# Kernel optimization log

Measured on AMD Instinct MI355X. Metric: run time of the kernel, lower is better.

Reference implementation:

```python
import jax, jax.numpy as jnp
import numpy as np


def setup_inputs() -> dict:
    key = jax.random.key(0)
    kA, kJ, kB, kP, kM = jax.random.split(key, 5)
    b, h, s = 4, 16, 1024
    A = jax.random.normal(kA, (b, h, s, s), dtype=jnp.float32)
    J = jax.random.normal(kJ, (b, h, s, s), dtype=jnp.float32)
    B = jax.random.normal(kB, (b, h, s, s), dtype=jnp.float32)
    P = jax.random.normal(kP, (b, h, s, s), dtype=jnp.float32)
    mask = jax.random.normal(kM, (1, s, s), dtype=jnp.float32)
    return {"A": A, "J": J, "B": B, "P": P, "mask": mask}


def reference(A, J, B, P, mask):
    # qk = A @ J + B, scaled by sqrt(last dim)
    s = A.shape[-1]
    scale = 1.0 / jnp.sqrt(jnp.asarray(s, dtype=A.dtype))
    qk = (jnp.einsum('bhik,bhkj->bhij', A, J) + B) * scale
    # mask [1, S, S] broadcasts over batch and heads, as in the torch source
    qk = qk + mask
    attn = jax.nn.softmax(qk, axis=-1)
    return jnp.einsum('bhij,bhjk->bhik', attn, P)
```

## Files before the change

### kernel.cpp

```cpp
#include <hip/hip_runtime.h>
#include <hip/hip_bf16.h>
#include <cstdint>


typedef __bf16 bf16x8 __attribute__((ext_vector_type(8)));
typedef __bf16 bf16x4 __attribute__((ext_vector_type(4)));
typedef float f32x4 __attribute__((ext_vector_type(4)));

static constexpr int SS = 1024;
static constexpr int BH = 64;
static constexpr size_t SLICE = (size_t)SS * SS;

__device__ __forceinline__ void async16(void* lds, const void* g) {
    __builtin_amdgcn_global_load_lds(
        (__attribute__((address_space(1))) void*)(g),
        (__attribute__((address_space(3))) void*)(lds), 16, 0, 0);
}

__global__ __launch_bounds__(256) void cast_bf16(const float4* __restrict__ in,
                                                 bf16x4* __restrict__ out, int n4) {
    int i = blockIdx.x * 256 + threadIdx.x;
    if (i < n4) {
        float4 v = in[i];
        bf16x4 o = {(__bf16)v.x, (__bf16)v.y, (__bf16)v.z, (__bf16)v.w};
        out[i] = o;
    }
}

__global__ __launch_bounds__(256) void transpose_cast(const float* __restrict__ in,
                                                      __bf16* __restrict__ out) {
    __shared__ float tile[32][33];
    const int bh = blockIdx.z;
    const int r0 = blockIdx.y * 32, c0 = blockIdx.x * 32;
    const int t = threadIdx.x;
    const int tr = t >> 3, tc4 = (t & 7) * 4;
    const float4 v = *(const float4*)(in + (size_t)bh * SLICE + (size_t)(r0 + tr) * SS + c0 + tc4);
    tile[tr][tc4 + 0] = v.x;
    tile[tr][tc4 + 1] = v.y;
    tile[tr][tc4 + 2] = v.z;
    tile[tr][tc4 + 3] = v.w;
    __syncthreads();
    const int oc = t >> 3;
    const int orr = (t & 7) * 4;
    bf16x4 o = {(__bf16)tile[orr + 0][oc], (__bf16)tile[orr + 1][oc],
                (__bf16)tile[orr + 2][oc], (__bf16)tile[orr + 3][oc]};
    *(bf16x4*)(out + (size_t)bh * SLICE + (size_t)(c0 + oc) * SS + r0 + orr) = o;
}


__global__ __launch_bounds__(256) void gemm_scores(const __bf16* __restrict__ Ab,
                                                   const __bf16* __restrict__ Jt,
                                                   const float* __restrict__ Bm,
                                                   const float* __restrict__ mask,
                                                   float* __restrict__ scores) {
    __shared__ __align__(16) __bf16 As[128 * 32];
    __shared__ __align__(16) __bf16 Bs[128 * 32];
    const int tid = threadIdx.x, lane = tid & 63, w = tid >> 6;
    const int wm = w >> 1, wn = w & 1;
    const int l16 = lane & 15, l4 = lane >> 4;
    const int bh = blockIdx.z;
    const int i0 = blockIdx.y * 128, j0 = blockIdx.x * 128;
    const size_t bhoff = (size_t)bh * SLICE;

    const __bf16* Ag = Ab + bhoff + (size_t)(i0 + w * 32 + (lane >> 2)) * SS + (lane & 3) * 8;
    const __bf16* Bg = Jt + bhoff + (size_t)(j0 + w * 32 + (lane >> 2)) * SS + (lane & 3) * 8;
    char* lA0 = (char*)As + w * 2048 + lane * 16;
    char* lB0 = (char*)Bs + w * 2048 + lane * 16;
    const __bf16* ar = As + (wm * 64 + l16) * 32 + l4 * 8;
    const __bf16* br = Bs + (wn * 64 + l16) * 32 + l4 * 8;

    f32x4 acc[4][4] = {};
    for (int kt = 0; kt < SS / 32; ++kt) {
        async16(lA0, Ag); async16(lA0 + 1024, Ag + 16 * SS);
        async16(lB0, Bg); async16(lB0 + 1024, Bg + 16 * SS);
        Ag += 32; Bg += 32;
        __syncthreads();
        bf16x8 af[4], bfr[4];
#pragma unroll
        for (int mi = 0; mi < 4; ++mi) af[mi] = *(const bf16x8*)(ar + mi * 16 * 32);
#pragma unroll
        for (int ni = 0; ni < 4; ++ni) bfr[ni] = *(const bf16x8*)(br + ni * 16 * 32);
#pragma unroll
        for (int mi = 0; mi < 4; ++mi)
#pragma unroll
            for (int ni = 0; ni < 4; ++ni)
                acc[mi][ni] = __builtin_amdgcn_mfma_f32_16x16x32_bf16(af[mi], bfr[ni], acc[mi][ni], 0, 0, 0);
        __syncthreads();
    }
    const float sc = 0.03125f;
#pragma unroll
    for (int mi = 0; mi < 4; ++mi) {
#pragma unroll
        for (int r = 0; r < 4; ++r) {
            const int ig = i0 + wm * 64 + mi * 16 + l4 * 4 + r;
#pragma unroll
            for (int ni = 0; ni < 4; ++ni) {
                const int jg = j0 + wn * 64 + ni * 16 + l16;
                const size_t off = bhoff + (size_t)ig * SS + jg;
                scores[off] = (acc[mi][ni][r] + Bm[off]) * sc + mask[(size_t)ig * SS + jg];
            }
        }
    }
}

__global__ __launch_bounds__(256) void gemm_out(const __bf16* __restrict__ At,
                                                const __bf16* __restrict__ Pt,
                                                float* __restrict__ out) {
    __shared__ __align__(16) __bf16 As[128 * 32];
    __shared__ __align__(16) __bf16 Bs[128 * 32];
    const int tid = threadIdx.x, lane = tid & 63, w = tid >> 6;
    const int wm = w >> 1, wn = w & 1;
    const int l16 = lane & 15, l4 = lane >> 4;
    const int bh = blockIdx.z;
    const int i0 = blockIdx.y * 128, j0 = blockIdx.x * 128;
    const size_t bhoff = (size_t)bh * SLICE;

    const __bf16* Ag = At + bhoff + (size_t)(i0 + w * 32 + (lane >> 2)) * SS + (lane & 3) * 8;
    const __bf16* Bg = Pt + bhoff + (size_t)(j0 + w * 32 + (lane >> 2)) * SS + (lane & 3) * 8;
    char* lA0 = (char*)As + w * 2048 + lane * 16;
    char* lB0 = (char*)Bs + w * 2048 + lane * 16;
    const __bf16* ar = As + (wm * 64 + l16) * 32 + l4 * 8;
    const __bf16* br = Bs + (wn * 64 + l16) * 32 + l4 * 8;

    f32x4 acc[4][4] = {};
    for (int kt = 0; kt < SS / 32; ++kt) {
        async16(lA0, Ag); async16(lA0 + 1024, Ag + 16 * SS);
        async16(lB0, Bg); async16(lB0 + 1024, Bg + 16 * SS);
        Ag += 32; Bg += 32;
        __syncthreads();
        bf16x8 af[4], bfr[4];
#pragma unroll
        for (int mi = 0; mi < 4; ++mi) af[mi] = *(const bf16x8*)(ar + mi * 16 * 32);
#pragma unroll
        for (int ni = 0; ni < 4; ++ni) bfr[ni] = *(const bf16x8*)(br + ni * 16 * 32);
#pragma unroll
        for (int mi = 0; mi < 4; ++mi)
#pragma unroll
            for (int ni = 0; ni < 4; ++ni)
                acc[mi][ni] = __builtin_amdgcn_mfma_f32_16x16x32_bf16(af[mi], bfr[ni], acc[mi][ni], 0, 0, 0);
        __syncthreads();
    }
#pragma unroll
    for (int mi = 0; mi < 4; ++mi) {
#pragma unroll
        for (int r = 0; r < 4; ++r) {
            const int ig = i0 + wm * 64 + mi * 16 + l4 * 4 + r;
#pragma unroll
            for (int ni = 0; ni < 4; ++ni) {
                const int jg = j0 + wn * 64 + ni * 16 + l16;
                out[bhoff + (size_t)ig * SS + jg] = acc[mi][ni][r];
            }
        }
    }
}

__global__ __launch_bounds__(256) void softmax_rows(const float* __restrict__ scores,
                                                    __bf16* __restrict__ attn) {
    const size_t row = blockIdx.x;
    const int t = threadIdx.x;
    const int lane = t & 63, w = t >> 6;
    __shared__ float red[8];

    float4 v = *(const float4*)(scores + row * SS + t * 4);
    float m = fmaxf(fmaxf(v.x, v.y), fmaxf(v.z, v.w));
#pragma unroll
    for (int o = 32; o; o >>= 1) m = fmaxf(m, __shfl_down(m, o));
    if (lane == 0) red[w] = m;
    __syncthreads();
    const float bm = fmaxf(fmaxf(red[0], red[1]), fmaxf(red[2], red[3]));
    const float e0 = __expf(v.x - bm), e1 = __expf(v.y - bm);
    const float e2 = __expf(v.z - bm), e3 = __expf(v.w - bm);
    float s = e0 + e1 + e2 + e3;
#pragma unroll
    for (int o = 32; o; o >>= 1) s += __shfl_down(s, o);
    __syncthreads();
    if (lane == 0) red[4 + w] = s;
    __syncthreads();
    const float inv = 1.0f / (red[4] + red[5] + red[6] + red[7]);
    bf16x4 o = {(__bf16)(e0 * inv), (__bf16)(e1 * inv), (__bf16)(e2 * inv), (__bf16)(e3 * inv)};
    *(bf16x4*)(attn + row * SS + t * 4) = o;
}

extern "C" void kernel_launch(void* const* d_in, const int* in_sizes, int n_in,
                              void* d_out, int out_size, void* d_ws, size_t ws_size,
                              hipStream_t stream) {
    const float* A    = (const float*)d_in[0];
    const float* J    = (const float*)d_in[1];
    const float* Bm   = (const float*)d_in[2];
    const float* P    = (const float*)d_in[3];
    const float* mask = (const float*)d_in[4];
    float* out = (float*)d_out;

    char* ws = (char*)d_ws;
    const size_t MB128 = (size_t)128 * 1024 * 1024;
    __bf16* Ab   = (__bf16*)ws;
    __bf16* Jt   = (__bf16*)(ws + MB128);
    __bf16* Pt   = (__bf16*)(ws + 2 * MB128);
    float*  scr  = (float*)(ws + 3 * MB128);
    __bf16* attn = Ab;

    const int n4 = (int)(BH * SLICE / 4);
    cast_bf16<<<dim3(n4 / 256), dim3(256), 0, stream>>>((const float4*)A, (bf16x4*)Ab, n4);
    transpose_cast<<<dim3(32, 32, BH), dim3(256), 0, stream>>>(J, Jt);
    transpose_cast<<<dim3(32, 32, BH), dim3(256), 0, stream>>>(P, Pt);
    gemm_scores<<<dim3(8, 8, BH), dim3(256), 0, stream>>>(Ab, Jt, Bm, mask, scr);
    softmax_rows<<<dim3(BH * SS), dim3(256), 0, stream>>>(scr, attn);
    gemm_out<<<dim3(8, 8, BH), dim3(256), 0, stream>>>(attn, Pt, out);
}
```

Measured before the change: 1.508 ms.

## Fuse score GEMM, softmax and output GEMM into one row-block kernel

Replaces the cast, scores GEMM, softmax and output GEMM kernels with one fused kernel per 32-row block. The kernel casts A into swizzled LDS, computes full 1024-wide score rows across 8 waves, reduces max and sum through LDS, writes exp values back to LDS as bf16, then multiplies by P and normalises at the end. This removes the fp32 score buffer round trip and the separate A cast pass. In exchange, J and P fragments are read straight from global memory with no LDS staging, so each block streams whole J and P slices, which leans heavily on L2 reuse.

```diff
diff --git a/kernel.cpp b/kernel.cpp
--- a/kernel.cpp
+++ b/kernel.cpp
@@ -10,22 +10,6 @@
 static constexpr int SS = 1024;
 static constexpr int BH = 64;
 static constexpr size_t SLICE = (size_t)SS * SS;
-
-__device__ __forceinline__ void async16(void* lds, const void* g) {
-    __builtin_amdgcn_global_load_lds(
-        (__attribute__((address_space(1))) void*)(g),
-        (__attribute__((address_space(3))) void*)(lds), 16, 0, 0);
-}
-
-__global__ __launch_bounds__(256) void cast_bf16(const float4* __restrict__ in,
-                                                 bf16x4* __restrict__ out, int n4) {
-    int i = blockIdx.x * 256 + threadIdx.x;
-    if (i < n4) {
-        float4 v = in[i];
-        bf16x4 o = {(__bf16)v.x, (__bf16)v.y, (__bf16)v.z, (__bf16)v.w};
-        out[i] = o;
-    }
-}
 
 __global__ __launch_bounds__(256) void transpose_cast(const float* __restrict__ in,
                                                       __bf16* __restrict__ out) {
@@ -47,138 +31,197 @@
     *(bf16x4*)(out + (size_t)bh * SLICE + (size_t)(c0 + oc) * SS + r0 + orr) = o;
 }
 
-
-__global__ __launch_bounds__(256) void gemm_scores(const __bf16* __restrict__ Ab,
-                                                   const __bf16* __restrict__ Jt,
-                                                   const float* __restrict__ Bm,
-                                                   const float* __restrict__ mask,
-                                                   float* __restrict__ scores) {
-    __shared__ __align__(16) __bf16 As[128 * 32];
-    __shared__ __align__(16) __bf16 Bs[128 * 32];
-    const int tid = threadIdx.x, lane = tid & 63, w = tid >> 6;
-    const int wm = w >> 1, wn = w & 1;
-    const int l16 = lane & 15, l4 = lane >> 4;
-    const int bh = blockIdx.z;
-    const int i0 = blockIdx.y * 128, j0 = blockIdx.x * 128;
+__global__ __launch_bounds__(512, 2) void fused_attn(
+    const float* __restrict__ A, const __bf16* __restrict__ Jt,
+    const float* __restrict__ Bm, const __bf16* __restrict__ Pt,
+    const float* __restrict__ mask, float* __restrict__ out) {
+
+    __shared__ __align__(16) char smem[64 * 1024 + 2048];
+    float* statM = (float*)(smem + 64 * 1024);
+    float* statS = statM + 256;
+
+    const int raw = (int)blockIdx.x;
+    const int lid = (raw & 7) * 256 + (raw >> 3);
+    const int bh  = lid >> 5;
+    const int i0  = (lid & 31) * 32;
     const size_t bhoff = (size_t)bh * SLICE;
 
-    const __bf16* Ag = Ab + bhoff + (size_t)(i0 + w * 32 + (lane >> 2)) * SS + (lane & 3) * 8;
-    const __bf16* Bg = Jt + bhoff + (size_t)(j0 + w * 32 + (lane >> 2)) * SS + (lane & 3) * 8;
-    char* lA0 = (char*)As + w * 2048 + lane * 16;
-    char* lB0 = (char*)Bs + w * 2048 + lane * 16;
-    const __bf16* ar = As + (wm * 64 + l16) * 32 + l4 * 8;
-    const __bf16* br = Bs + (wn * 64 + l16) * 32 + l4 * 8;
-
-    f32x4 acc[4][4] = {};
-    for (int kt = 0; kt < SS / 32; ++kt) {
-        async16(lA0, Ag); async16(lA0 + 1024, Ag + 16 * SS);
-        async16(lB0, Bg); async16(lB0 + 1024, Bg + 16 * SS);
-        Ag += 32; Bg += 32;
-        __syncthreads();
-        bf16x8 af[4], bfr[4];
-#pragma unroll
-        for (int mi = 0; mi < 4; ++mi) af[mi] = *(const bf16x8*)(ar + mi * 16 * 32);
-#pragma unroll
-        for (int ni = 0; ni < 4; ++ni) bfr[ni] = *(const bf16x8*)(br + ni * 16 * 32);
-#pragma unroll
-        for (int mi = 0; mi < 4; ++mi)
-#pragma unroll
-            for (int ni = 0; ni < 4; ++ni)
-                acc[mi][ni] = __builtin_amdgcn_mfma_f32_16x16x32_bf16(af[mi], bfr[ni], acc[mi][ni], 0, 0, 0);
-        __syncthreads();
-    }
-    const float sc = 0.03125f;
-#pragma unroll
-    for (int mi = 0; mi < 4; ++mi) {
-#pragma unroll
-        for (int r = 0; r < 4; ++r) {
-            const int ig = i0 + wm * 64 + mi * 16 + l4 * 4 + r;
-#pragma unroll
-            for (int ni = 0; ni < 4; ++ni) {
-                const int jg = j0 + wn * 64 + ni * 16 + l16;
-                const size_t off = bhoff + (size_t)ig * SS + jg;
-                scores[off] = (acc[mi][ni][r] + Bm[off]) * sc + mask[(size_t)ig * SS + jg];
-            }
-        }
-    }
-}
-
-__global__ __launch_bounds__(256) void gemm_out(const __bf16* __restrict__ At,
-                                                const __bf16* __restrict__ Pt,
-                                                float* __restrict__ out) {
-    __shared__ __align__(16) __bf16 As[128 * 32];
-    __shared__ __align__(16) __bf16 Bs[128 * 32];
-    const int tid = threadIdx.x, lane = tid & 63, w = tid >> 6;
-    const int wm = w >> 1, wn = w & 1;
-    const int l16 = lane & 15, l4 = lane >> 4;
-    const int bh = blockIdx.z;
-    const int i0 = blockIdx.y * 128, j0 = blockIdx.x * 128;
-    const size_t bhoff = (size_t)bh * SLICE;
-
-    const __bf16* Ag = At + bhoff + (size_t)(i0 + w * 32 + (lane >> 2)) * SS + (lane & 3) * 8;
-    const __bf16* Bg = Pt + bhoff + (size_t)(j0 + w * 32 + (lane >> 2)) * SS + (lane & 3) * 8;
-    char* lA0 = (char*)As + w * 2048 + lane * 16;
-    char* lB0 = (char*)Bs + w * 2048 + lane * 16;
-    const __bf16* ar = As + (wm * 64 + l16) * 32 + l4 * 8;
-    const __bf16* br = Bs + (wn * 64 + l16) * 32 + l4 * 8;
-
-    f32x4 acc[4][4] = {};
-    for (int kt = 0; kt < SS / 32; ++kt) {
-        async16(lA0, Ag); async16(lA0 + 1024, Ag + 16 * SS);
-        async16(lB0, Bg); async16(lB0 + 1024, Bg + 16 * SS);
-        Ag += 32; Bg += 32;
-        __syncthreads();
-        bf16x8 af[4], bfr[4];
-#pragma unroll
-        for (int mi = 0; mi < 4; ++mi) af[mi] = *(const bf16x8*)(ar + mi * 16 * 32);
-#pragma unroll
-        for (int ni = 0; ni < 4; ++ni) bfr[ni] = *(const bf16x8*)(br + ni * 16 * 32);
-#pragma unroll
-        for (int mi = 0; mi < 4; ++mi)
-#pragma unroll
-            for (int ni = 0; ni < 4; ++ni)
-                acc[mi][ni] = __builtin_amdgcn_mfma_f32_16x16x32_bf16(af[mi], bfr[ni], acc[mi][ni], 0, 0, 0);
-        __syncthreads();
-    }
-#pragma unroll
-    for (int mi = 0; mi < 4; ++mi) {
-#pragma unroll
-        for (int r = 0; r < 4; ++r) {
-            const int ig = i0 + wm * 64 + mi * 16 + l4 * 4 + r;
-#pragma unroll
-            for (int ni = 0; ni < 4; ++ni) {
-                const int jg = j0 + wn * 64 + ni * 16 + l16;
-                out[bhoff + (size_t)ig * SS + jg] = acc[mi][ni][r];
-            }
-        }
-    }
-}
-
-__global__ __launch_bounds__(256) void softmax_rows(const float* __restrict__ scores,
-                                                    __bf16* __restrict__ attn) {
-    const size_t row = blockIdx.x;
-    const int t = threadIdx.x;
-    const int lane = t & 63, w = t >> 6;
-    __shared__ float red[8];
-
-    float4 v = *(const float4*)(scores + row * SS + t * 4);
-    float m = fmaxf(fmaxf(v.x, v.y), fmaxf(v.z, v.w));
-#pragma unroll
-    for (int o = 32; o; o >>= 1) m = fmaxf(m, __shfl_down(m, o));
-    if (lane == 0) red[w] = m;
-    __syncthreads();
-    const float bm = fmaxf(fmaxf(red[0], red[1]), fmaxf(red[2], red[3]));
-    const float e0 = __expf(v.x - bm), e1 = __expf(v.y - bm);
-    const float e2 = __expf(v.z - bm), e3 = __expf(v.w - bm);
-    float s = e0 + e1 + e2 + e3;
-#pragma unroll
-    for (int o = 32; o; o >>= 1) s += __shfl_down(s, o);
-    __syncthreads();
-    if (lane == 0) red[4 + w] = s;
-    __syncthreads();
-    const float inv = 1.0f / (red[4] + red[5] + red[6] + red[7]);
-    bf16x4 o = {(__bf16)(e0 * inv), (__bf16)(e1 * inv), (__bf16)(e2 * inv), (__bf16)(e3 * inv)};
-    *(bf16x4*)(attn + row * SS + t * 4) = o;
+    const int tid  = threadIdx.x;
+    const int lane = tid & 63, w = tid >> 6;
+    const int l16  = lane & 15, l4 = lane >> 4;
+    const int jw   = w * 128;
+    const int sw   = (l16 & 7) << 4;
+
+    {
+        const float* Ab = A + bhoff + (size_t)i0 * SS;
+#pragma unroll
+        for (int c = 0; c < 16; ++c) {
+            const int elem = c * 2048 + tid * 4;
+            const int row = elem >> 10;
+            const int colb = (elem & 1023) * 2;
+            const float4 v = *(const float4*)(Ab + elem);
+            bf16x4 o = {(__bf16)v.x, (__bf16)v.y, (__bf16)v.z, (__bf16)v.w};
+            *(bf16x4*)(smem + row * 2048 + (colb ^ ((row & 7) << 4))) = o;
+        }
+    }
+    __syncthreads();
+
+    f32x4 acc[2][8] = {};
+    {
+        const __bf16* Jg = Jt + bhoff + (size_t)(jw + l16) * SS + l4 * 8;
+        const char* a0 = smem + l16 * 2048;
+        const char* a1 = smem + (16 + l16) * 2048;
+#pragma unroll 2
+        for (int kt = 0; kt < 32; ++kt) {
+            bf16x8 bfr[8];
+#pragma unroll
+            for (int ni = 0; ni < 8; ++ni)
+                bfr[ni] = *(const bf16x8*)(Jg + (size_t)ni * 16 * SS + kt * 32);
+            const int ko = (kt * 64 + l4 * 16) ^ sw;
+            bf16x8 af0 = *(const bf16x8*)(a0 + ko);
+            bf16x8 af1 = *(const bf16x8*)(a1 + ko);
+#pragma unroll
+            for (int ni = 0; ni < 8; ++ni) {
+                acc[0][ni] = __builtin_amdgcn_mfma_f32_16x16x32_bf16(af0, bfr[ni], acc[0][ni], 0, 0, 0);
+                acc[1][ni] = __builtin_amdgcn_mfma_f32_16x16x32_bf16(af1, bfr[ni], acc[1][ni], 0, 0, 0);
+            }
+        }
+    }
+
+    const float scl = 0.03125f;
+    float rm[2][4];
+#pragma unroll
+    for (int mi = 0; mi < 2; ++mi)
+#pragma unroll
+        for (int r = 0; r < 4; ++r) rm[mi][r] = -3.4e38f;
+#pragma unroll
+    for (int mi = 0; mi < 2; ++mi) {
+#pragma unroll
+        for (int r = 0; r < 4; ++r) {
+            const int ig = i0 + mi * 16 + l4 * 4 + r;
+#pragma unroll
+            for (int ni = 0; ni < 8; ++ni) {
+                const int jg = jw + ni * 16 + l16;
+                float v = (acc[mi][ni][r] + Bm[bhoff + (size_t)ig * SS + jg]) * scl
+                          + mask[(size_t)ig * SS + jg];
+                acc[mi][ni][r] = v;
+                rm[mi][r] = fmaxf(rm[mi][r], v);
+            }
+        }
+    }
+#pragma unroll
+    for (int mi = 0; mi < 2; ++mi)
+#pragma unroll
+        for (int r = 0; r < 4; ++r) {
+            float m = rm[mi][r];
+            m = fmaxf(m, __shfl_xor(m, 1));
+            m = fmaxf(m, __shfl_xor(m, 2));
+            m = fmaxf(m, __shfl_xor(m, 4));
+            m = fmaxf(m, __shfl_xor(m, 8));
+            rm[mi][r] = m;
+        }
+    if (l16 == 0) {
+#pragma unroll
+        for (int mi = 0; mi < 2; ++mi)
+#pragma unroll
+            for (int r = 0; r < 4; ++r)
+                statM[w * 32 + mi * 16 + l4 * 4 + r] = rm[mi][r];
+    }
+    __syncthreads();
+
+    float gm[2][4], ls[2][4];
+#pragma unroll
+    for (int mi = 0; mi < 2; ++mi)
+#pragma unroll
+        for (int r = 0; r < 4; ++r) {
+            const int rowi = mi * 16 + l4 * 4 + r;
+            float g = statM[rowi];
+#pragma unroll
+            for (int ww = 1; ww < 8; ++ww) g = fmaxf(g, statM[ww * 32 + rowi]);
+            gm[mi][r] = g;
+            ls[mi][r] = 0.f;
+        }
+
+#pragma unroll
+    for (int mi = 0; mi < 2; ++mi) {
+#pragma unroll
+        for (int r = 0; r < 4; ++r) {
+            const int rowi = mi * 16 + l4 * 4 + r;
+            const int swr = (rowi & 7) << 4;
+#pragma unroll
+            for (int ni = 0; ni < 8; ++ni) {
+                const int jl = jw + ni * 16 + l16;
+                float e = __expf(acc[mi][ni][r] - gm[mi][r]);
+                ls[mi][r] += e;
+                *(__bf16*)(smem + rowi * 2048 + ((jl * 2) ^ swr)) = (__bf16)e;
+            }
+        }
+    }
+#pragma unroll
+    for (int mi = 0; mi < 2; ++mi)
+#pragma unroll
+        for (int r = 0; r < 4; ++r) {
+            float s = ls[mi][r];
+            s += __shfl_xor(s, 1);
+            s += __shfl_xor(s, 2);
+            s += __shfl_xor(s, 4);
+            s += __shfl_xor(s, 8);
+            ls[mi][r] = s;
+        }
+    if (l16 == 0) {
+#pragma unroll
+        for (int mi = 0; mi < 2; ++mi)
+#pragma unroll
+            for (int r = 0; r < 4; ++r)
+                statS[w * 32 + mi * 16 + l4 * 4 + r] = ls[mi][r];
+    }
+    __syncthreads();
+
+    float inv[2][4];
+#pragma unroll
+    for (int mi = 0; mi < 2; ++mi)
+#pragma unroll
+        for (int r = 0; r < 4; ++r) {
+            const int rowi = mi * 16 + l4 * 4 + r;
+            float s = statS[rowi];
+#pragma unroll
+            for (int ww = 1; ww < 8; ++ww) s += statS[ww * 32 + rowi];
+            inv[mi][r] = 1.0f / s;
+        }
+
+    f32x4 oac[2][8] = {};
+    {
+        const __bf16* Pg = Pt + bhoff + (size_t)(jw + l16) * SS + l4 * 8;
+        const char* a0 = smem + l16 * 2048;
+        const char* a1 = smem + (16 + l16) * 2048;
+#pragma unroll 2
+        for (int kt = 0; kt < 32; ++kt) {
+            bf16x8 pfr[8];
+#pragma unroll
+            for (int ni = 0; ni < 8; ++ni)
+                pfr[ni] = *(const bf16x8*)(Pg + (size_t)ni * 16 * SS + kt * 32);
+            const int ko = (kt * 64 + l4 * 16) ^ sw;
+            bf16x8 af0 = *(const bf16x8*)(a0 + ko);
+            bf16x8 af1 = *(const bf16x8*)(a1 + ko);
+#pragma unroll
+            for (int ni = 0; ni < 8; ++ni) {
+                oac[0][ni] = __builtin_amdgcn_mfma_f32_16x16x32_bf16(af0, pfr[ni], oac[0][ni], 0, 0, 0);
+                oac[1][ni] = __builtin_amdgcn_mfma_f32_16x16x32_bf16(af1, pfr[ni], oac[1][ni], 0, 0, 0);
+            }
+        }
+    }
+
+#pragma unroll
+    for (int mi = 0; mi < 2; ++mi)
+#pragma unroll
+        for (int r = 0; r < 4; ++r) {
+            const int ig = i0 + mi * 16 + l4 * 4 + r;
+#pragma unroll
+            for (int ni = 0; ni < 8; ++ni) {
+                const int ng = jw + ni * 16 + l16;
+                out[bhoff + (size_t)ig * SS + ng] = oac[mi][ni][r] * inv[mi][r];
+            }
+        }
 }
 
 extern "C" void kernel_launch(void* const* d_in, const int* in_sizes, int n_in,
@@ -193,17 +236,10 @@
 
     char* ws = (char*)d_ws;
     const size_t MB128 = (size_t)128 * 1024 * 1024;
-    __bf16* Ab   = (__bf16*)ws;
-    __bf16* Jt   = (__bf16*)(ws + MB128);
-    __bf16* Pt   = (__bf16*)(ws + 2 * MB128);
-    float*  scr  = (float*)(ws + 3 * MB128);
-    __bf16* attn = Ab;
-
-    const int n4 = (int)(BH * SLICE / 4);
-    cast_bf16<<<dim3(n4 / 256), dim3(256), 0, stream>>>((const float4*)A, (bf16x4*)Ab, n4);
+    __bf16* Jt = (__bf16*)ws;
+    __bf16* Pt = (__bf16*)(ws + MB128);
+
     transpose_cast<<<dim3(32, 32, BH), dim3(256), 0, stream>>>(J, Jt);
     transpose_cast<<<dim3(32, 32, BH), dim3(256), 0, stream>>>(P, Pt);
-    gemm_scores<<<dim3(8, 8, BH), dim3(256), 0, stream>>>(Ab, Jt, Bm, mask, scr);
-    softmax_rows<<<dim3(BH * SS), dim3(256), 0, stream>>>(scr, attn);
-    gemm_out<<<dim3(8, 8, BH), dim3(256), 0, stream>>>(attn, Pt, out);
+    fused_attn<<<dim3(BH * 32), dim3(512), 0, stream>>>(A, Jt, Bm, Pt, mask, out);
 }
```

Result: slower. 2.270 ms (+50.5%).
